# Kernel optimization log

Measured on AMD Instinct MI355X. Metric: run time of the kernel, lower is better.

The kernel has to match this reference:

```python
import jax, jax.numpy as jnp
import numpy as np

B, Q, HID = 2, 2048, 2048
HQ, HKV, D = 16, 4, 128
EPS = 1e-6
THETA = 1000000.0


def _rmsnorm(x, w):
    # x: [..., D]
    return x * jax.lax.rsqrt(jnp.mean(x * x, axis=-1, keepdims=True) + EPS) * w


def _rope(x, cos, sin):
    # neox-style: split halves. x: [B,Q,H,D], cos/sin: [B,Q,1,D/2]
    d2 = x.shape[-1] // 2
    x1, x2 = x[..., :d2], x[..., d2:]
    return jnp.concatenate([x1 * cos - x2 * sin, x2 * cos + x1 * sin], axis=-1)


def setup_inputs() -> dict:
    key = jax.random.key(0)
    k1, k2, k3 = jax.random.split(key, 3)
    positions = jnp.broadcast_to(jnp.arange(Q, dtype=jnp.int32), (B, Q))
    hidden_states = jax.random.normal(k1, (B, Q, HID), dtype=jnp.float32)
    k_cache = jnp.zeros((B, HKV, Q, D), dtype=jnp.float32)
    v_cache = jnp.zeros((B, HKV, Q, D), dtype=jnp.float32)
    wqkv = jax.random.normal(k2, (HQ * D + 2 * HKV * D, HID), dtype=jnp.float32) * (HID ** -0.5)
    wo = jax.random.normal(k3, (HID, HQ * D), dtype=jnp.float32) * ((HQ * D) ** -0.5)
    q_norm_w = jnp.ones((D,), dtype=jnp.float32)
    k_norm_w = jnp.ones((D,), dtype=jnp.float32)
    return {"positions": positions, "hidden_states": hidden_states, "k_cache": k_cache,
            "v_cache": v_cache, "wqkv": wqkv, "wo": wo, "q_norm_w": q_norm_w,
            "k_norm_w": k_norm_w, "seq_len": Q}


def reference(positions, hidden_states, k_cache, v_cache, wqkv, wo, q_norm_w, k_norm_w, seq_len):
    bsz, qlen, _ = hidden_states.shape
    q_size, kv_size = HQ * D, HKV * D
    scale = D ** -0.5

    qkv = hidden_states.reshape(bsz * qlen, HID) @ wqkv.T  # [B*Q, q+2kv]
    q = qkv[:, :q_size].reshape(bsz, qlen, HQ, D)
    k = qkv[:, q_size:q_size + kv_size].reshape(bsz, qlen, HKV, D)
    v = qkv[:, q_size + kv_size:].reshape(bsz, qlen, HKV, D)

    q = _rmsnorm(q, q_norm_w)
    k = _rmsnorm(k, k_norm_w)

    inv_freq = 1.0 / (THETA ** (jnp.arange(0, D, 2, dtype=jnp.float32) / D))  # [D/2]
    freqs = positions.astype(jnp.float32)[..., None] * inv_freq  # [B,Q,D/2]
    cos = jnp.cos(freqs)[:, :, None, :]
    sin = jnp.sin(freqs)[:, :, None, :]
    q = _rope(q, cos, sin)
    k = _rope(k, cos, sin)

    q = q.transpose(0, 2, 1, 3)  # [B,HQ,Q,D]
    k = k.transpose(0, 2, 1, 3)  # [B,HKV,Q,D]
    v = v.transpose(0, 2, 1, 3)

    start = seq_len - qlen
    k_cache = jax.lax.dynamic_update_slice(k_cache, k, (0, 0, start, 0))
    v_cache = jax.lax.dynamic_update_slice(v_cache, v, (0, 0, start, 0))
    k_full = k_cache[:, :, :seq_len, :]
    v_full = v_cache[:, :, :seq_len, :]

    rep = HQ // HKV
    kf = jnp.repeat(k_full, rep, axis=1)  # [B,HQ,S,D]
    vf = jnp.repeat(v_full, rep, axis=1)

    scores = jnp.einsum('bhqd,bhkd->bhqk', q, kf) * scale
    if qlen == seq_len:  # is_causal path
        causal = jnp.tril(jnp.ones((qlen, seq_len), dtype=bool))
        scores = jnp.where(causal, scores, jnp.finfo(scores.dtype).min)
    attn = jax.nn.softmax(scores, axis=-1)
    out = jnp.einsum('bhqk,bhkd->bhqd', attn, vf)  # [B,HQ,Q,D]
    out = out.transpose(0, 2, 1, 3).reshape(bsz * qlen, HQ * D)
    return (out @ wo.T).reshape(bsz, qlen, HID)
```

## Files before the change

kernel.cpp:

```cpp
#include <hip/hip_runtime.h>

#define B_    2
#define Q_    2048
#define HID_  2048
#define HQ_   16
#define HKV_  4
#define D_    128
#define QSC_  (0.08838834764831843f * 1.4426950408889634f)
#define LOG2_THETA 19.931568569324174f
#define FMAX_ 20.0f

typedef unsigned short u16;
typedef __attribute__((ext_vector_type(8))) short bf16x8;
typedef __attribute__((ext_vector_type(4))) float f32x4;

__device__ __forceinline__ u16 f2bf(float x) {
  union { float f; unsigned int u; } v; v.f = x;
  unsigned int r = v.u + 0x7FFFu + ((v.u >> 16) & 1u);
  return (u16)(r >> 16);
}
__device__ __forceinline__ u16 f2bf_t(float x) {
  union { float f; unsigned int u; } v; v.f = x;
  return (u16)(v.u >> 16);
}

__device__ __forceinline__ void gl2lds16(u16* lds, const u16* g) {
  __builtin_amdgcn_global_load_lds((const __attribute__((address_space(1))) void*)g,
                                   (__attribute__((address_space(3))) void*)lds,
                                   16, 0, 0);
}

#define N4_HID  2097152
#define N4_WQKV 1572864
#define N4_WO   1048576
#define N4_ALL  (N4_HID + N4_WQKV + N4_WO)
#define NROPE   (B_ * Q_ * 64)
__global__ __launch_bounds__(256) void cvt_all(const float* __restrict__ h,
                                               const float* __restrict__ wq,
                                               const float* __restrict__ wo,
                                               const int* __restrict__ pos,
                                               u16* __restrict__ oh,
                                               u16* __restrict__ owq,
                                               u16* __restrict__ owo,
                                               float* __restrict__ rope) {
  int i = blockIdx.x * 256 + threadIdx.x;
  if (i >= N4_ALL) {
    int j = i - N4_ALL;
    int d = j & 63, row = j >> 6;
    float p = (float)pos[row];
    float inv = exp2f(-(float)d * (LOG2_THETA / 64.f));
    float sn, cn;
    sincosf(p * inv, &sn, &cn);
    ((float2*)rope)[j] = make_float2(cn, sn);
    return;
  }
  const float* src; u16* dst; int off;
  if (i < N4_HID)                 { src = h;  dst = oh;  off = i; }
  else if (i < N4_HID + N4_WQKV)  { src = wq; dst = owq; off = i - N4_HID; }
  else                            { src = wo; dst = owo; off = i - N4_HID - N4_WQKV; }
  float4 v = *(const float4*)(src + (size_t)off * 4);
  ushort4 o;
  o.x = f2bf(v.x); o.y = f2bf(v.y); o.z = f2bf(v.z); o.w = f2bf(v.w);
  *(ushort4*)(dst + (size_t)off * 4) = o;
}

__global__ __launch_bounds__(512) void gemm_qkv8(const u16* __restrict__ A,
                                                 const u16* __restrict__ Bw,
                                                 const float* __restrict__ rope,
                                                 const float* __restrict__ qw,
                                                 const float* __restrict__ kw,
                                                 u16* __restrict__ qb,
                                                 u16* __restrict__ kb,
                                                 u16* __restrict__ vt) {
  __shared__ __align__(16) u16 lds[65536];
  const int tid = threadIdx.x;
  const int wv = tid >> 6, lane = tid & 63;
  const int wm = wv >> 1, wn = wv & 1;
  const int c = lane & 15, quad = lane >> 4;
  const int m0 = blockIdx.x * 256;
  const int by = blockIdx.y;
  const int n0 = by * 256;
  const int xg = ((lane & 7) ^ (lane >> 3)) * 8;
  const int x0 = ((quad)     ^ (c & 7)) * 8;
  const int x1 = ((quad | 4) ^ (c & 7)) * 8;
  const int aoff = (wm >> 1) * 8192 + (wm & 1) * 4096 + c * 64;
  const int boff = 32768 + wn * 8192 + c * 64;
  const u16* Ag = A  + (size_t)m0 * HID_;
  const u16* Bg = Bw + (size_t)n0 * HID_;
  const int NIT = HID_ >> 7;

#define STGQ(base, g, h, kt, buf)                                             \
  { _Pragma("unroll")                                                         \
    for (int j = 0; j < 2; ++j) {                                             \
      const int s = j * 8 + wv;                                               \
      gl2lds16(lds + (base) + (buf) * 16384 + (h) * 8192 + s * 512,           \
               (g) + (size_t)((h) * 128 + s * 8 + (lane >> 3)) * HID_         \
                   + (kt) * 64 + xg);                                         \
    } }
#define STGQ_A(h, kt, buf) STGQ(0,     Ag, h, kt, buf)
#define STGQ_B(h, kt, buf) STGQ(32768, Bg, h, kt, buf)
#define BARQ()  asm volatile("s_barrier" ::: "memory")
#define WLGQ()  { asm volatile("s_waitcnt lgkmcnt(0)" ::: "memory");          \
                  __builtin_amdgcn_sched_barrier(0); }
#define WVMQ(n) { asm volatile("s_waitcnt vmcnt(" #n ")" ::: "memory");       \
                  __builtin_amdgcn_sched_barrier(0); }
#define MMQ(MF, NF, FA, MI) {                                                 \
  acc[MF][NF] = __builtin_amdgcn_mfma_f32_16x16x32_bf16(FA[MI][0], fB[(NF)&3][0], \
                                                        acc[MF][NF], 0, 0, 0);\
  acc[MF][NF] = __builtin_amdgcn_mfma_f32_16x16x32_bf16(FA[MI][1], fB[(NF)&3][1], \
                                                        acc[MF][NF], 0, 0, 0); }

  f32x4 acc[4][8] = {};
  bf16x8 fAa[2][2], fAb[2][2], fB[4][2];

  STGQ_A(0, 0, 0); STGQ_A(1, 0, 0); STGQ_B(0, 0, 0); STGQ_B(1, 0, 0);
  STGQ_A(0, 1, 1); STGQ_B(0, 1, 1);
  WVMQ(4);
  BARQ();

#pragma unroll 1
  for (int it = 0; it < NIT; ++it) {
    const bool last = (it == NIT - 1);
    const int kt1 = 2 * it + 1, kt2 = 2 * it + 2, kt3 = 2 * it + 3;

#pragma unroll
    for (int mi = 0; mi < 2; ++mi) {
      fAa[mi][0] = *(const bf16x8*)(lds + aoff + mi * 1024 + x0);
      fAa[mi][1] = *(const bf16x8*)(lds + aoff + mi * 1024 + x1);
    }
#pragma unroll
    for (int nf = 0; nf < 4; ++nf) {
      fB[nf][0] = *(const bf16x8*)(lds + boff + nf * 1024 + x0);
      fB[nf][1] = *(const bf16x8*)(lds + boff + nf * 1024 + x1);
    }
    STGQ_A(1, kt1, 1);
    BARQ(); WLGQ();
    __builtin_amdgcn_s_setprio(1);
#pragma unroll
    for (int mi = 0; mi < 2; ++mi)
#pragma unroll
      for (int nf = 0; nf < 4; ++nf) MMQ(mi, nf, fAa, mi);
    __builtin_amdgcn_s_setprio(0);
    BARQ();

#pragma unroll
    for (int mi = 0; mi < 2; ++mi) {
      fAb[mi][0] = *(const bf16x8*)(lds + aoff + (2 + mi) * 1024 + x0);
      fAb[mi][1] = *(const bf16x8*)(lds + aoff + (2 + mi) * 1024 + x1);
    }
    STGQ_B(1, kt1, 1);
    BARQ(); WLGQ();
    __builtin_amdgcn_s_setprio(1);
#pragma unroll
    for (int mi = 0; mi < 2; ++mi)
#pragma unroll
      for (int nf = 0; nf < 4; ++nf) MMQ(2 + mi, nf, fAb, mi);
    __builtin_amdgcn_s_setprio(0);
    BARQ();

#pragma unroll
    for (int nf = 0; nf < 4; ++nf) {
      fB[nf][0] = *(const bf16x8*)(lds + boff + (4 + nf) * 1024 + x0);
      fB[nf][1] = *(const bf16x8*)(lds + boff + (4 + nf) * 1024 + x1);
    }
    if (!last) STGQ_A(0, kt2, 0);
    BARQ(); WLGQ();
    __builtin_amdgcn_s_setprio(1);
#pragma unroll
    for (int mi = 0; mi < 2; ++mi)
#pragma unroll
      for (int nf = 4; nf < 8; ++nf) MMQ(2 + mi, nf, fAb, mi);
    __builtin_amdgcn_s_setprio(0);
    BARQ();

    if (!last) STGQ_B(0, kt2, 0);
    BARQ(); WLGQ();
    __builtin_amdgcn_s_setprio(1);
#pragma unroll
    for (int mi = 0; mi < 2; ++mi)
#pragma unroll
      for (int nf = 4; nf < 8; ++nf) MMQ(mi, nf, fAa, mi);
    __builtin_amdgcn_s_setprio(0);
    if (last) { WVMQ(0); } else { WVMQ(4); }
    BARQ();

#pragma unroll
    for (int mi = 0; mi < 2; ++mi) {
      fAa[mi][0] = *(const bf16x8*)(lds + 16384 + aoff + mi * 1024 + x0);
      fAa[mi][1] = *(const bf16x8*)(lds + 16384 + aoff + mi * 1024 + x1);
    }
#pragma unroll
    for (int nf = 0; nf < 4; ++nf) {
      fB[nf][0] = *(const bf16x8*)(lds + 16384 + boff + nf * 1024 + x0);
      fB[nf][1] = *(const bf16x8*)(lds + 16384 + boff + nf * 1024 + x1);
    }
    if (!last) STGQ_A(1, kt2, 0);
    BARQ(); WLGQ();
    __builtin_amdgcn_s_setprio(1);
#pragma unroll
    for (int mi = 0; mi < 2; ++mi)
#pragma unroll
      for (int nf = 0; nf < 4; ++nf) MMQ(mi, nf, fAa, mi);
    __builtin_amdgcn_s_setprio(0);
    BARQ();

#pragma unroll
    for (int mi = 0; mi < 2; ++mi) {
      fAb[mi][0] = *(const bf16x8*)(lds + 16384 + aoff + (2 + mi) * 1024 + x0);
      fAb[mi][1] = *(const bf16x8*)(lds + 16384 + aoff + (2 + mi) * 1024 + x1);
    }
    if (!last) STGQ_B(1, kt2, 0);
    BARQ(); WLGQ();
    __builtin_amdgcn_s_setprio(1);
#pragma unroll
    for (int mi = 0; mi < 2; ++mi)
#pragma unroll
      for (int nf = 0; nf < 4; ++nf) MMQ(2 + mi, nf, fAb, mi);
    __builtin_amdgcn_s_setprio(0);
    BARQ();

#pragma unroll
    for (int nf = 0; nf < 4; ++nf) {
      fB[nf][0] = *(const bf16x8*)(lds + 16384 + boff + (4 + nf) * 1024 + x0);
      fB[nf][1] = *(const bf16x8*)(lds + 16384 + boff + (4 + nf) * 1024 + x1);
    }
    if (!last) STGQ_A(0, kt3, 1);
    BARQ(); WLGQ();
    __builtin_amdgcn_s_setprio(1);
#pragma unroll
    for (int mi = 0; mi < 2; ++mi)
#pragma unroll
      for (int nf = 4; nf < 8; ++nf) MMQ(2 + mi, nf, fAb, mi);
    __builtin_amdgcn_s_setprio(0);
    BARQ();

    if (!last) STGQ_B(0, kt3, 1);
    BARQ(); WLGQ();
    __builtin_amdgcn_s_setprio(1);
#pragma unroll
    for (int mi = 0; mi < 2; ++mi)
#pragma unroll
      for (int nf = 4; nf < 8; ++nf) MMQ(mi, nf, fAa, mi);
    __builtin_amdgcn_s_setprio(0);
    if (last) { WVMQ(0); } else { WVMQ(4); }
    BARQ();
  }

  const int h = by * 2 + wn;
  if (h < 20) {
    const bool isq = h < 16;
    const float* w = isq ? qw : kw;
    const float osc = isq ? QSC_ : 1.f;
    float wl[8];
#pragma unroll
    for (int nf = 0; nf < 8; ++nf) wl[nf] = w[nf * 16 + c];
    u16* dstbuf = isq ? qb : kb;
    const int hbase = isq ? h : (h - 16);
    const int nheads = isq ? HQ_ : HKV_;
    u16* lw = lds + wv * 4224;
#pragma unroll
    for (int pass = 0; pass < 2; ++pass) {
#pragma unroll
      for (int mi = 0; mi < 2; ++mi) {
        const int mf = pass * 2 + mi;
#pragma unroll
        for (int r = 0; r < 4; ++r) {
          const int row = m0 + wm * 64 + mf * 16 + quad * 4 + r;
          const int q = row & (Q_ - 1), b = row >> 11;
          float ss = 0.f;
#pragma unroll
          for (int nf = 0; nf < 8; ++nf) ss += acc[mf][nf][r] * acc[mf][nf][r];
          ss += __shfl_xor(ss, 1); ss += __shfl_xor(ss, 2);
          ss += __shfl_xor(ss, 4); ss += __shfl_xor(ss, 8);
          const float rn = rsqrtf(ss * (1.f / 128.f) + 1e-6f) * osc;
          u16* lrow = lw + (mi * 16 + quad * 4 + r) * 132;
#pragma unroll
          for (int ni = 0; ni < 4; ni++) {
            float2 cssn = *(const float2*)(rope +
                ((size_t)(b * Q_ + q) * 64 + ni * 16 + c) * 2);
            float x1 = acc[mf][ni][r]     * wl[ni]     * rn;
            float x2 = acc[mf][ni + 4][r] * wl[ni + 4] * rn;
            lrow[ni * 16 + c]       = f2bf(x1 * cssn.x - x2 * cssn.y);
            lrow[(ni + 4) * 16 + c] = f2bf(x2 * cssn.x + x1 * cssn.y);
          }
        }
      }
#pragma unroll
      for (int itr = 0; itr < 8; ++itr) {
        const int rl = itr * 4 + quad;
        const int rowg = m0 + wm * 64 + pass * 32 + rl;
        const int q = rowg & (Q_ - 1), b = rowg >> 11;
        u16* dst = dstbuf + (((size_t)(b * nheads) + hbase) * Q_ + q) * D_ + c * 8;
        *(bf16x8*)dst = *(const bf16x8*)(lw + rl * 132 + c * 8);
      }
    }
  } else {
    const int hk = h - 20;
    const int bb = m0 >> 11;
    const int q0w = (m0 & (Q_ - 1)) + wm * 64;
    u16* lw = lds + wv * 4352;
#pragma unroll
    for (int pass = 0; pass < 2; ++pass) {
#pragma unroll
      for (int nfl = 0; nfl < 4; ++nfl) {
        const int nf = pass * 4 + nfl;
#pragma unroll
        for (int mf = 0; mf < 4; ++mf) {
          short4 pv;
          pv.x = (short)f2bf(acc[mf][nf][0]); pv.y = (short)f2bf(acc[mf][nf][1]);
          pv.z = (short)f2bf(acc[mf][nf][2]); pv.w = (short)f2bf(acc[mf][nf][3]);
          *(short4*)(lw + (nfl * 16 + c) * 68 + mf * 16 + quad * 4) = pv;
        }
      }
#pragma unroll
      for (int itr = 0; itr < 8; ++itr) {
        const int dl = itr * 8 + (lane >> 3);
        const int d = pass * 64 + dl;
        u16* dst = vt + (((size_t)(bb * HKV_) + hk) * D_ + d) * Q_ +
                   q0w + (lane & 7) * 8;
        *(bf16x8*)dst = *(const bf16x8*)(lw + dl * 68 + (lane & 7) * 8);
      }
    }
  }
#undef STGQ
#undef STGQ_A
#undef STGQ_B
#undef BARQ
#undef WLGQ
#undef WVMQ
#undef MMQ
}

__global__ __launch_bounds__(512) void gemm_bt8(const u16* __restrict__ A,
                                                const u16* __restrict__ Bw,
                                                float* __restrict__ C,
                                                int M, int N, int K) {
  __shared__ __align__(16) u16 lds[49152];
  const int tid = threadIdx.x;
  const int wv = tid >> 6, lane = tid & 63;
  const int wm = wv >> 2, wn = wv & 3;
  const int c = lane & 15, quad = lane >> 4;
  const int m0 = blockIdx.x * 128, n0 = blockIdx.y * 256;
  const int xg = ((lane & 7) ^ (lane >> 3)) * 8;
  const int x0 = ((quad)     ^ (c & 7)) * 8;
  const int x1 = ((quad | 4) ^ (c & 7)) * 8;
  const int aoff = wm * 4096 + c * 64;
  const int boff = 16384 + (wn >> 1) * 8192 + (wn & 1) * 4096 + c * 64;
  const u16* Ag = A  + (size_t)m0 * K;
  const u16* Bg = Bw + (size_t)n0 * K;
  const int NIT = K >> 7;

#define STA2(h, kt, buf)                                                      \
  gl2lds16(lds + (buf) * 8192 + (h) * 4096 + wv * 512,                        \
           Ag + (size_t)((h) * 64 + wv * 8 + (lane >> 3)) * K + (kt) * 64 + xg);
#define STB2(h, kt, buf)                                                      \
  { _Pragma("unroll")                                                         \
    for (int j = 0; j < 2; ++j)                                               \
      gl2lds16(lds + 16384 + (buf) * 16384 + (h) * 8192 + j * 4096 + wv * 512,\
               Bg + (size_t)((h) * 128 + j * 64 + wv * 8 + (lane >> 3)) * K   \
                   + (kt) * 64 + xg); }
#define BAR8()  asm volatile("s_barrier" ::: "memory")
#define WLG8()  { asm volatile("s_waitcnt lgkmcnt(0)" ::: "memory");          \
                  __builtin_amdgcn_sched_barrier(0); }
#define WVM8(n) { asm volatile("s_waitcnt vmcnt(" #n ")" ::: "memory");       \
                  __builtin_amdgcn_sched_barrier(0); }
#define MM2(MF, NF, FA, FB, MI, NI) {                                         \
  acc[MF][NF] = __builtin_amdgcn_mfma_f32_16x16x32_bf16(FA[MI][0], FB[NI][0], \
                                                        acc[MF][NF], 0, 0, 0);\
  acc[MF][NF] = __builtin_amdgcn_mfma_f32_16x16x32_bf16(FA[MI][1], FB[NI][1], \
                                                        acc[MF][NF], 0, 0, 0); }

  f32x4 acc[4][4] = {};
  bf16x8 fAa[2][2], fAb[2][2], fBa[2][2], fBb[2][2];

  STA2(0, 0, 0); STA2(1, 0, 0); STB2(0, 0, 0); STB2(1, 0, 0);
  STA2(0, 1, 1); STA2(1, 1, 1); STB2(0, 1, 1); STB2(1, 1, 1);
  WVM8(6);
  BAR8();

#pragma unroll 1
  for (int it = 0; it < NIT; ++it) {
    const bool last = (it == NIT - 1);
    const int kt2 = 2 * it + 2, kt3 = 2 * it + 3;

#pragma unroll
    for (int mi = 0; mi < 2; ++mi) {
      fAa[mi][0] = *(const bf16x8*)(lds + aoff + mi * 1024 + x0);
      fAa[mi][1] = *(const bf16x8*)(lds + aoff + mi * 1024 + x1);
      fBa[mi][0] = *(const bf16x8*)(lds + boff + mi * 1024 + x0);
      fBa[mi][1] = *(const bf16x8*)(lds + boff + mi * 1024 + x1);
    }
    BAR8(); WLG8();
    __builtin_amdgcn_s_setprio(1);
    MM2(0, 0, fAa, fBa, 0, 0); MM2(0, 1, fAa, fBa, 0, 1);
    MM2(1, 0, fAa, fBa, 1, 0); MM2(1, 1, fAa, fBa, 1, 1);
    __builtin_amdgcn_s_setprio(0);
    BAR8();

#pragma unroll
    for (int mi = 0; mi < 2; ++mi) {
      fAb[mi][0] = *(const bf16x8*)(lds + aoff + (2 + mi) * 1024 + x0);
      fAb[mi][1] = *(const bf16x8*)(lds + aoff + (2 + mi) * 1024 + x1);
    }
    BAR8(); WLG8();
    __builtin_amdgcn_s_setprio(1);
    MM2(2, 0, fAb, fBa, 0, 0); MM2(2, 1, fAb, fBa, 0, 1);
    MM2(3, 0, fAb, fBa, 1, 0); MM2(3, 1, fAb, fBa, 1, 1);
    __builtin_amdgcn_s_setprio(0);
    BAR8();

#pragma unroll
    for (int ni = 0; ni < 2; ++ni) {
      fBb[ni][0] = *(const bf16x8*)(lds + boff + (2 + ni) * 1024 + x0);
      fBb[ni][1] = *(const bf16x8*)(lds + boff + (2 + ni) * 1024 + x1);
    }
    if (!last) { STA2(0, kt2, 0); STA2(1, kt2, 0); }
    BAR8(); WLG8();
    __builtin_amdgcn_s_setprio(1);
    MM2(2, 2, fAb, fBb, 0, 0); MM2(2, 3, fAb, fBb, 0, 1);
    MM2(3, 2, fAb, fBb, 1, 0); MM2(3, 3, fAb, fBb, 1, 1);
    __builtin_amdgcn_s_setprio(0);
    BAR8();

    if (!last) { STB2(0, kt2, 0); STB2(1, kt2, 0); }
    BAR8(); WLG8();
    __builtin_amdgcn_s_setprio(1);
    MM2(0, 2, fAa, fBb, 0, 0); MM2(0, 3, fAa, fBb, 0, 1);
    MM2(1, 2, fAa, fBb, 1, 0); MM2(1, 3, fAa, fBb, 1, 1);
    __builtin_amdgcn_s_setprio(0);
    if (last) { WVM8(0); } else { WVM8(6); }
    BAR8();

#pragma unroll
    for (int mi = 0; mi < 2; ++mi) {
      fAa[mi][0] = *(const bf16x8*)(lds + 8192 + aoff + mi * 1024 + x0);
      fAa[mi][1] = *(const bf16x8*)(lds + 8192 + aoff + mi * 1024 + x1);
      fBa[mi][0] = *(const bf16x8*)(lds + 16384 + boff + mi * 1024 + x0);
      fBa[mi][1] = *(const bf16x8*)(lds + 16384 + boff + mi * 1024 + x1);
    }
    BAR8(); WLG8();
    __builtin_amdgcn_s_setprio(1);
    MM2(0, 0, fAa, fBa, 0, 0); MM2(0, 1, fAa, fBa, 0, 1);
    MM2(1, 0, fAa, fBa, 1, 0); MM2(1, 1, fAa, fBa, 1, 1);
    __builtin_amdgcn_s_setprio(0);
    BAR8();

#pragma unroll
    for (int mi = 0; mi < 2; ++mi) {
      fAb[mi][0] = *(const bf16x8*)(lds + 8192 + aoff + (2 + mi) * 1024 + x0);
      fAb[mi][1] = *(const bf16x8*)(lds + 8192 + aoff + (2 + mi) * 1024 + x1);
    }
    BAR8(); WLG8();
    __builtin_amdgcn_s_setprio(1);
    MM2(2, 0, fAb, fBa, 0, 0); MM2(2, 1, fAb, fBa, 0, 1);
    MM2(3, 0, fAb, fBa, 1, 0); MM2(3, 1, fAb, fBa, 1, 1);
    __builtin_amdgcn_s_setprio(0);
    BAR8();

#pragma unroll
    for (int ni = 0; ni < 2; ++ni) {
      fBb[ni][0] = *(const bf16x8*)(lds + 16384 + boff + (2 + ni) * 1024 + x0);
      fBb[ni][1] = *(const bf16x8*)(lds + 16384 + boff + (2 + ni) * 1024 + x1);
    }
    if (!last) { STA2(0, kt3, 1); STA2(1, kt3, 1); }
    BAR8(); WLG8();
    __builtin_amdgcn_s_setprio(1);
    MM2(2, 2, fAb, fBb, 0, 0); MM2(2, 3, fAb, fBb, 0, 1);
    MM2(3, 2, fAb, fBb, 1, 0); MM2(3, 3, fAb, fBb, 1, 1);
    __builtin_amdgcn_s_setprio(0);
    BAR8();

    if (!last) { STB2(0, kt3, 1); STB2(1, kt3, 1); }
    BAR8(); WLG8();
    __builtin_amdgcn_s_setprio(1);
    MM2(0, 2, fAa, fBb, 0, 0); MM2(0, 3, fAa, fBb, 0, 1);
    MM2(1, 2, fAa, fBb, 1, 0); MM2(1, 3, fAa, fBb, 1, 1);
    __builtin_amdgcn_s_setprio(0);
    if (last) { WVM8(0); } else { WVM8(6); }
    BAR8();
  }

  const int crow = m0 + wm * 64 + quad * 4;
  const int ccol = n0 + wn * 64 + c;
#pragma unroll
  for (int mf = 0; mf < 4; ++mf)
#pragma unroll
    for (int nf = 0; nf < 4; ++nf)
#pragma unroll
      for (int r = 0; r < 4; ++r)
        C[(size_t)(crow + mf * 16 + r) * N + ccol + nf * 16] = acc[mf][nf][r];
#undef STA2
#undef STB2
#undef BAR8
#undef WLG8
#undef WVM8
#undef MM2
}

__global__ __launch_bounds__(256) void attn_fwd(const u16* __restrict__ qb,
                                                const u16* __restrict__ kb,
                                                const u16* __restrict__ vt,
                                                u16* __restrict__ ob) {
  __shared__ __align__(16) u16 lds[32768 + 8192];
  const int p = blockIdx.x, h = blockIdx.y, b = blockIdx.z;
  const int hk = h >> 2;
  const int tid = threadIdx.x, wave = tid >> 6, lane = tid & 63;
  const int c = lane & 15, quad = lane >> 4;
  const int lr = lane >> 2, lp = lane & 3;
  const int lpg = (lp + 4 - ((lr >> 1) & 3)) & 3;
  const int swq = ((quad + (c >> 1)) & 3) * 8;
  const int psw = (c & 7) << 3;
  const u16* qg = qb + ((size_t)b * HQ_ + h) * (size_t)Q_ * D_;
  const u16* kg = kb + ((size_t)b * HKV_ + hk) * (size_t)Q_ * D_;
  const u16* vg = vt + ((size_t)b * HKV_ + hk) * (size_t)D_ * Q_;
  u16* Pw = lds + 32768 + wave * 2048;
  u16* Bw = lds + wave * 2176;

#define ASTAGE(KT, BS)                                                        \
  { _Pragma("unroll")                                                         \
    for (int i = 0; i < 4; i++) {                                             \
      gl2lds16(lds + (BS) * 8192 + (size_t)(i * 256 + wave * 64) * 8,         \
               kg + ((size_t)(KT) * 64 + wave * 16 + lr) * D_ + i * 32 + lpg * 8); \
      int d = (i & 1) * 64 + wave * 16 + lr;                                  \
      gl2lds16(lds + 16384 + (BS) * 8192 + (size_t)(i * 256 + wave * 64) * 8, \
               vg + (size_t)d * Q_ + (KT) * 64 + (i >> 1) * 32 + lpg * 8);    \
    } }
#define MFMA_A(A0, B0, C0) __builtin_amdgcn_mfma_f32_16x16x32_bf16(A0, B0, C0, 0, 0, 0)

#pragma unroll 1
  for (int tp = 0; tp < 2; tp++) {
    const int t = tp ? (15 - p) : p;
    const int q0 = t * 128;
    const int qbase = q0 + wave * 32;
    bf16x8 qf[2][4];
#pragma unroll
    for (int qh = 0; qh < 2; qh++)
#pragma unroll
      for (int kk = 0; kk < 4; kk++)
        qf[qh][kk] = *(const bf16x8*)(qg + (size_t)(qbase + qh * 16 + c) * D_ +
                                      kk * 32 + quad * 8);
    f32x4 Oa[8][2] = {};
    float l0 = 0.f, l1 = 0.f;

    if (tp) __syncthreads();
    ASTAGE(0, 0);

    const int nkt = 2 * t + 2;
#pragma unroll 1
    for (int kt = 0; kt < nkt; kt++) {
      const int bs = kt & 1;
      __syncthreads();
      if (kt < nkt - 1) ASTAGE(kt + 1, bs ^ 1);
      const u16* Ksb = lds + bs * 8192;
      const u16* Vsb = lds + 16384 + bs * 8192;
      f32x4 S[4][2];
#pragma unroll
      for (int n = 0; n < 4; n++) {
        S[n][0] = f32x4{-FMAX_, -FMAX_, -FMAX_, -FMAX_};
        S[n][1] = f32x4{-FMAX_, -FMAX_, -FMAX_, -FMAX_};
#pragma unroll
        for (int kk = 0; kk < 4; kk++) {
          bf16x8 kf = *(const bf16x8*)(Ksb + kk * 2048 + (n * 16 + c) * 32 + swq);
          S[n][0] = MFMA_A(kf, qf[0][kk], S[n][0]);
          S[n][1] = MFMA_A(kf, qf[1][kk], S[n][1]);
        }
      }
      if (kt >= 2 * t) {
#pragma unroll
        for (int n = 0; n < 4; n++)
#pragma unroll
          for (int qh = 0; qh < 2; qh++)
#pragma unroll
            for (int r = 0; r < 4; r++) {
              int key = kt * 64 + n * 16 + quad * 4 + r;
              if (key > qbase + qh * 16 + c) S[n][qh][r] = -1e9f;
            }
      }
#pragma unroll
      for (int n = 0; n < 4; n++)
#pragma unroll
        for (int qh = 0; qh < 2; qh++) {
          float p0 = __builtin_amdgcn_exp2f(S[n][qh][0]);
          float p1 = __builtin_amdgcn_exp2f(S[n][qh][1]);
          float p2 = __builtin_amdgcn_exp2f(S[n][qh][2]);
          float p3 = __builtin_amdgcn_exp2f(S[n][qh][3]);
          if (qh) l1 += (p0 + p1) + (p2 + p3);
          else    l0 += (p0 + p1) + (p2 + p3);
          short4 pk;
          pk.x = (short)f2bf_t(p0); pk.y = (short)f2bf_t(p1);
          pk.z = (short)f2bf_t(p2); pk.w = (short)f2bf_t(p3);
          *(short4*)(Pw + (qh * 16 + c) * 64 + ((n * 16 + quad * 4) ^ psw)) = pk;
        }
      bf16x8 pf[2][2];
#pragma unroll
      for (int qh = 0; qh < 2; qh++)
#pragma unroll
        for (int kk2 = 0; kk2 < 2; kk2++)
          pf[qh][kk2] = *(const bf16x8*)(Pw + (qh * 16 + c) * 64 +
                                         ((kk2 * 32 + quad * 8) ^ psw));
#pragma unroll
      for (int md = 0; md < 8; md++)
#pragma unroll
        for (int kk2 = 0; kk2 < 2; kk2++) {
          bf16x8 vf = *(const bf16x8*)(Vsb + kk2 * 4096 + (md * 16 + c) * 32 + swq);
          Oa[md][0] = MFMA_A(vf, pf[0][kk2], Oa[md][0]);
          Oa[md][1] = MFMA_A(vf, pf[1][kk2], Oa[md][1]);
        }
    }
    l0 += __shfl_xor(l0, 16); l0 += __shfl_xor(l0, 32);
    l1 += __shfl_xor(l1, 16); l1 += __shfl_xor(l1, 32);
    __syncthreads();
#pragma unroll
    for (int qh = 0; qh < 2; qh++) {
      const float invl = 1.f / (qh ? l1 : l0);
#pragma unroll
      for (int md = 0; md < 8; md++) {
        short4 ok;
        ok.x = (short)f2bf(Oa[md][qh][0] * invl);
        ok.y = (short)f2bf(Oa[md][qh][1] * invl);
        ok.z = (short)f2bf(Oa[md][qh][2] * invl);
        ok.w = (short)f2bf(Oa[md][qh][3] * invl);
        *(short4*)(Bw + c * 136 + md * 16 + quad * 4) = ok;
      }
      const int orow = q0 + wave * 32 + qh * 16 + lr;
#pragma unroll
      for (int tt = 0; tt < 4; tt++) {
        bf16x8 ov = *(const bf16x8*)(Bw + lr * 136 + lp * 32 + tt * 8);
        *(bf16x8*)(ob + ((size_t)(b * Q_ + orow) * HQ_ + h) * D_ + lp * 32 + tt * 8) = ov;
      }
      asm volatile("s_waitcnt lgkmcnt(0)" ::: "memory");
      __builtin_amdgcn_sched_barrier(0);
    }
  }
#undef ASTAGE
#undef MFMA_A
}

extern "C" void kernel_launch(void* const* d_in, const int* in_sizes, int n_in,
                              void* d_out, int out_size, void* d_ws, size_t ws_size,
                              hipStream_t stream) {
  const int*   positions = (const int*)  d_in[0];
  const float* hidden    = (const float*)d_in[1];
  const float* wqkv      = (const float*)d_in[4];
  const float* wo        = (const float*)d_in[5];
  const float* qnw       = (const float*)d_in[6];
  const float* knw       = (const float*)d_in[7];
  char* ws = (char*)d_ws;
  u16*   hid_bf  = (u16*)(ws);
  u16*   wqkv_bf = (u16*)(ws + 16777216);
  u16*   wo_bf   = (u16*)(ws + 29360128);
  u16*   q_bf    = (u16*)(ws + 37748736);
  u16*   k_bf    = (u16*)(ws + 54525952);
  u16*   vt_bf   = (u16*)(ws + 58720256);
  float* rope    = (float*)(ws + 62914560);
  u16*   attn_bf = hid_bf;

  cvt_all<<<19456, 256, 0, stream>>>(hidden, wqkv, wo, positions,
                                     hid_bf, wqkv_bf, wo_bf, rope);
  gemm_qkv8<<<dim3(16, 12), 512, 0, stream>>>(hid_bf, wqkv_bf, rope, qnw, knw,
                                              q_bf, k_bf, vt_bf);
  attn_fwd<<<dim3(8, 16, 2), 256, 0, stream>>>(q_bf, k_bf, vt_bf, attn_bf);
  gemm_bt8<<<dim3(32, 8), 512, 0, stream>>>(attn_bf, wo_bf, (float*)d_out,
                                            4096, 2048, 2048);
}
```

Baseline: 289.6 us.

## Prefetch K/V through registers with single LDS buffer, one tile per block

The attention kernel now launches one block per 128-row query tile, with heavy tiles scheduled first, instead of pairing a light and a heavy tile in each block. The double-buffered direct global-to-LDS staging is replaced by a register prefetch of the next K/V tile that is written into a single LDS buffer at the top of each iteration. This halves LDS use, which may allow more resident blocks, and doubles the grid so the causal load can balance dynamically. The cost is extra VGPRs for the prefetch registers and a second barrier per iteration.

After: 306.6 us. 1.06x slower.

```diff
diff --git a/kernel.cpp b/kernel.cpp
--- a/kernel.cpp
+++ b/kernel.cpp
@@ -501,8 +501,9 @@
                                                 const u16* __restrict__ kb,
                                                 const u16* __restrict__ vt,
                                                 u16* __restrict__ ob) {
-  __shared__ __align__(16) u16 lds[32768 + 8192];
-  const int p = blockIdx.x, h = blockIdx.y, b = blockIdx.z;
+  __shared__ __align__(16) u16 lds[24576];
+  const int t = 15 - blockIdx.x;
+  const int h = blockIdx.y, b = blockIdx.z;
   const int hk = h >> 2;
   const int tid = threadIdx.x, wave = tid >> 6, lane = tid & 63;
   const int c = lane & 15, quad = lane >> 4;
@@ -513,126 +514,129 @@
   const u16* qg = qb + ((size_t)b * HQ_ + h) * (size_t)Q_ * D_;
   const u16* kg = kb + ((size_t)b * HKV_ + hk) * (size_t)Q_ * D_;
   const u16* vg = vt + ((size_t)b * HKV_ + hk) * (size_t)D_ * Q_;
-  u16* Pw = lds + 32768 + wave * 2048;
+  u16* Pw = lds + 16384 + wave * 2048;
   u16* Bw = lds + wave * 2176;
 
-#define ASTAGE(KT, BS)                                                        \
+#define GLDKV(KT)                                                             \
   { _Pragma("unroll")                                                         \
     for (int i = 0; i < 4; i++) {                                             \
-      gl2lds16(lds + (BS) * 8192 + (size_t)(i * 256 + wave * 64) * 8,         \
-               kg + ((size_t)(KT) * 64 + wave * 16 + lr) * D_ + i * 32 + lpg * 8); \
-      int d = (i & 1) * 64 + wave * 16 + lr;                                  \
-      gl2lds16(lds + 16384 + (BS) * 8192 + (size_t)(i * 256 + wave * 64) * 8, \
-               vg + (size_t)d * Q_ + (KT) * 64 + (i >> 1) * 32 + lpg * 8);    \
+      kreg[i] = *(const bf16x8*)(kg + ((size_t)(KT) * 64 + wave * 16 + lr) * D_ \
+                                 + i * 32 + lpg * 8);                         \
+      vreg[i] = *(const bf16x8*)(vg + (size_t)((i & 1) * 64 + wave * 16 + lr) * Q_ \
+                                 + (KT) * 64 + (i >> 1) * 32 + lpg * 8);      \
     } }
+#define BARA()  asm volatile("s_barrier" ::: "memory")
+#define WLGA()  { asm volatile("s_waitcnt lgkmcnt(0)" ::: "memory");          \
+                  __builtin_amdgcn_sched_barrier(0); }
 #define MFMA_A(A0, B0, C0) __builtin_amdgcn_mfma_f32_16x16x32_bf16(A0, B0, C0, 0, 0, 0)
 
+  const int q0 = t * 128;
+  const int qbase = q0 + wave * 32;
+  bf16x8 qf[2][4];
+#pragma unroll
+  for (int qh = 0; qh < 2; qh++)
+#pragma unroll
+    for (int kk = 0; kk < 4; kk++)
+      qf[qh][kk] = *(const bf16x8*)(qg + (size_t)(qbase + qh * 16 + c) * D_ +
+                                    kk * 32 + quad * 8);
+  f32x4 Oa[8][2] = {};
+  float l0 = 0.f, l1 = 0.f;
+  bf16x8 kreg[4], vreg[4];
+
+  GLDKV(0);
+  const int nkt = 2 * t + 2;
 #pragma unroll 1
-  for (int tp = 0; tp < 2; tp++) {
-    const int t = tp ? (15 - p) : p;
-    const int q0 = t * 128;
-    const int qbase = q0 + wave * 32;
-    bf16x8 qf[2][4];
+  for (int kt = 0; kt < nkt; kt++) {
+    BARA();
+#pragma unroll
+    for (int i = 0; i < 4; i++) {
+      *(bf16x8*)(lds + (size_t)(i * 256 + wave * 64 + lane) * 8) = kreg[i];
+      *(bf16x8*)(lds + 8192 + (size_t)(i * 256 + wave * 64 + lane) * 8) = vreg[i];
+    }
+    if (kt + 1 < nkt) GLDKV(kt + 1);
+    WLGA(); BARA();
+    f32x4 S[4][2];
+#pragma unroll
+    for (int n = 0; n < 4; n++) {
+      S[n][0] = f32x4{-FMAX_, -FMAX_, -FMAX_, -FMAX_};
+      S[n][1] = f32x4{-FMAX_, -FMAX_, -FMAX_, -FMAX_};
+#pragma unroll
+      for (int kk = 0; kk < 4; kk++) {
+        bf16x8 kf = *(const bf16x8*)(lds + kk * 2048 + (n * 16 + c) * 32 + swq);
+        S[n][0] = MFMA_A(kf, qf[0][kk], S[n][0]);
+        S[n][1] = MFMA_A(kf, qf[1][kk], S[n][1]);
+      }
+    }
+    if (kt >= 2 * t) {
+#pragma unroll
+      for (int n = 0; n < 4; n++)
+#pragma unroll
+        for (int qh = 0; qh < 2; qh++)
+#pragma unroll
+          for (int r = 0; r < 4; r++) {
+            int key = kt * 64 + n * 16 + quad * 4 + r;
+            if (key > qbase + qh * 16 + c) S[n][qh][r] = -1e9f;
+          }
+    }
+#pragma unroll
+    for (int n = 0; n < 4; n++)
+#pragma unroll
+      for (int qh = 0; qh < 2; qh++) {
+        float p0 = __builtin_amdgcn_exp2f(S[n][qh][0]);
+        float p1 = __builtin_amdgcn_exp2f(S[n][qh][1]);
+        float p2 = __builtin_amdgcn_exp2f(S[n][qh][2]);
+        float p3 = __builtin_amdgcn_exp2f(S[n][qh][3]);
+        if (qh) l1 += (p0 + p1) + (p2 + p3);
+        else    l0 += (p0 + p1) + (p2 + p3);
+        short4 pk;
+        pk.x = (short)f2bf_t(p0); pk.y = (short)f2bf_t(p1);
+        pk.z = (short)f2bf_t(p2); pk.w = (short)f2bf_t(p3);
+        *(short4*)(Pw + (qh * 16 + c) * 64 + ((n * 16 + quad * 4) ^ psw)) = pk;
+      }
+    bf16x8 pf[2][2];
 #pragma unroll
     for (int qh = 0; qh < 2; qh++)
 #pragma unroll
-      for (int kk = 0; kk < 4; kk++)
-        qf[qh][kk] = *(const bf16x8*)(qg + (size_t)(qbase + qh * 16 + c) * D_ +
-                                      kk * 32 + quad * 8);
-    f32x4 Oa[8][2] = {};
-    float l0 = 0.f, l1 = 0.f;
-
-    if (tp) __syncthreads();
-    ASTAGE(0, 0);
-
-    const int nkt = 2 * t + 2;
-#pragma unroll 1
-    for (int kt = 0; kt < nkt; kt++) {
-      const int bs = kt & 1;
-      __syncthreads();
-      if (kt < nkt - 1) ASTAGE(kt + 1, bs ^ 1);
-      const u16* Ksb = lds + bs * 8192;
-      const u16* Vsb = lds + 16384 + bs * 8192;
-      f32x4 S[4][2];
-#pragma unroll
-      for (int n = 0; n < 4; n++) {
-        S[n][0] = f32x4{-FMAX_, -FMAX_, -FMAX_, -FMAX_};
-        S[n][1] = f32x4{-FMAX_, -FMAX_, -FMAX_, -FMAX_};
-#pragma unroll
-        for (int kk = 0; kk < 4; kk++) {
-          bf16x8 kf = *(const bf16x8*)(Ksb + kk * 2048 + (n * 16 + c) * 32 + swq);
-          S[n][0] = MFMA_A(kf, qf[0][kk], S[n][0]);
-          S[n][1] = MFMA_A(kf, qf[1][kk], S[n][1]);
-        }
+      for (int kk2 = 0; kk2 < 2; kk2++)
+        pf[qh][kk2] = *(const bf16x8*)(Pw + (qh * 16 + c) * 64 +
+                                       ((kk2 * 32 + quad * 8) ^ psw));
+#pragma unroll
+    for (int md = 0; md < 8; md++)
+#pragma unroll
+      for (int kk2 = 0; kk2 < 2; kk2++) {
+        bf16x8 vf = *(const bf16x8*)(lds + 8192 + kk2 * 4096 +
+                                     (md * 16 + c) * 32 + swq);
+        Oa[md][0] = MFMA_A(vf, pf[0][kk2], Oa[md][0]);
+        Oa[md][1] = MFMA_A(vf, pf[1][kk2], Oa[md][1]);
       }
-      if (kt >= 2 * t) {
-#pragma unroll
-        for (int n = 0; n < 4; n++)
-#pragma unroll
-          for (int qh = 0; qh < 2; qh++)
-#pragma unroll
-            for (int r = 0; r < 4; r++) {
-              int key = kt * 64 + n * 16 + quad * 4 + r;
-              if (key > qbase + qh * 16 + c) S[n][qh][r] = -1e9f;
-            }
-      }
-#pragma unroll
-      for (int n = 0; n < 4; n++)
-#pragma unroll
-        for (int qh = 0; qh < 2; qh++) {
-          float p0 = __builtin_amdgcn_exp2f(S[n][qh][0]);
-          float p1 = __builtin_amdgcn_exp2f(S[n][qh][1]);
-          float p2 = __builtin_amdgcn_exp2f(S[n][qh][2]);
-          float p3 = __builtin_amdgcn_exp2f(S[n][qh][3]);
-          if (qh) l1 += (p0 + p1) + (p2 + p3);
-          else    l0 += (p0 + p1) + (p2 + p3);
-          short4 pk;
-          pk.x = (short)f2bf_t(p0); pk.y = (short)f2bf_t(p1);
-          pk.z = (short)f2bf_t(p2); pk.w = (short)f2bf_t(p3);
-          *(short4*)(Pw + (qh * 16 + c) * 64 + ((n * 16 + quad * 4) ^ psw)) = pk;
-        }
-      bf16x8 pf[2][2];
-#pragma unroll
-      for (int qh = 0; qh < 2; qh++)
-#pragma unroll
-        for (int kk2 = 0; kk2 < 2; kk2++)
-          pf[qh][kk2] = *(const bf16x8*)(Pw + (qh * 16 + c) * 64 +
-                                         ((kk2 * 32 + quad * 8) ^ psw));
-#pragma unroll
-      for (int md = 0; md < 8; md++)
-#pragma unroll
-        for (int kk2 = 0; kk2 < 2; kk2++) {
-          bf16x8 vf = *(const bf16x8*)(Vsb + kk2 * 4096 + (md * 16 + c) * 32 + swq);
-          Oa[md][0] = MFMA_A(vf, pf[0][kk2], Oa[md][0]);
-          Oa[md][1] = MFMA_A(vf, pf[1][kk2], Oa[md][1]);
-        }
-    }
-    l0 += __shfl_xor(l0, 16); l0 += __shfl_xor(l0, 32);
-    l1 += __shfl_xor(l1, 16); l1 += __shfl_xor(l1, 32);
-    __syncthreads();
-#pragma unroll
-    for (int qh = 0; qh < 2; qh++) {
-      const float invl = 1.f / (qh ? l1 : l0);
-#pragma unroll
-      for (int md = 0; md < 8; md++) {
-        short4 ok;
-        ok.x = (short)f2bf(Oa[md][qh][0] * invl);
-        ok.y = (short)f2bf(Oa[md][qh][1] * invl);
-        ok.z = (short)f2bf(Oa[md][qh][2] * invl);
-        ok.w = (short)f2bf(Oa[md][qh][3] * invl);
-        *(short4*)(Bw + c * 136 + md * 16 + quad * 4) = ok;
-      }
-      const int orow = q0 + wave * 32 + qh * 16 + lr;
-#pragma unroll
-      for (int tt = 0; tt < 4; tt++) {
-        bf16x8 ov = *(const bf16x8*)(Bw + lr * 136 + lp * 32 + tt * 8);
-        *(bf16x8*)(ob + ((size_t)(b * Q_ + orow) * HQ_ + h) * D_ + lp * 32 + tt * 8) = ov;
-      }
-      asm volatile("s_waitcnt lgkmcnt(0)" ::: "memory");
-      __builtin_amdgcn_sched_barrier(0);
-    }
   }
-#undef ASTAGE
+  l0 += __shfl_xor(l0, 16); l0 += __shfl_xor(l0, 32);
+  l1 += __shfl_xor(l1, 16); l1 += __shfl_xor(l1, 32);
+  WLGA(); BARA();
+#pragma unroll
+  for (int qh = 0; qh < 2; qh++) {
+    const float invl = 1.f / (qh ? l1 : l0);
+#pragma unroll
+    for (int md = 0; md < 8; md++) {
+      short4 ok;
+      ok.x = (short)f2bf(Oa[md][qh][0] * invl);
+      ok.y = (short)f2bf(Oa[md][qh][1] * invl);
+      ok.z = (short)f2bf(Oa[md][qh][2] * invl);
+      ok.w = (short)f2bf(Oa[md][qh][3] * invl);
+      *(short4*)(Bw + c * 136 + md * 16 + quad * 4) = ok;
+    }
+    const int orow = q0 + wave * 32 + qh * 16 + lr;
+#pragma unroll
+    for (int tt = 0; tt < 4; tt++) {
+      bf16x8 ov = *(const bf16x8*)(Bw + lr * 136 + lp * 32 + tt * 8);
+      *(bf16x8*)(ob + ((size_t)(b * Q_ + orow) * HQ_ + h) * D_ + lp * 32 + tt * 8) = ov;
+    }
+    asm volatile("s_waitcnt lgkmcnt(0)" ::: "memory");
+    __builtin_amdgcn_sched_barrier(0);
+  }
+#undef GLDKV
+#undef BARA
+#undef WLGA
 #undef MFMA_A
 }
 
@@ -659,7 +663,7 @@
                                      hid_bf, wqkv_bf, wo_bf, rope);
   gemm_qkv8<<<dim3(16, 12), 512, 0, stream>>>(hid_bf, wqkv_bf, rope, qnw, knw,
                                               q_bf, k_bf, vt_bf);
-  attn_fwd<<<dim3(8, 16, 2), 256, 0, stream>>>(q_bf, k_bf, vt_bf, attn_bf);
+  attn_fwd<<<dim3(16, 16, 2), 256, 0, stream>>>(q_bf, k_bf, vt_bf, attn_bf);
   gemm_bt8<<<dim3(32, 8), 512, 0, stream>>>(attn_bf, wo_bf, (float*)d_out,
                                             4096, 2048, 2048);
 }
```
